# Kernel optimization log

Measured on AMD Instinct MI355X. Metric: run time of the kernel, lower is better.

Reference implementation:

```python
import jax, jax.numpy as jnp
import numpy as np

B, S, D = 32, 8192, 64


def setup_inputs() -> dict:
    key = jax.random.key(0)
    k1, k2 = jax.random.split(key)
    input_real = jax.random.normal(k1, (B, S, D), dtype=jnp.float32)
    input_imag = jax.random.normal(k2, (B, S, D), dtype=jnp.float32)
    return {"input_real": input_real, "input_imag": input_imag}


def reference(input_real, input_imag):
    # ComplexMixture: mean over seq of per-token complex outer products v v^H.
    # Original builds [B,S,D,D] via 4 batch_dots then means over S; fused here
    # as Gram contractions over the sequence axis (no [B,S,D,D] intermediate).
    seq_len = input_real.shape[1]
    inv_s = jnp.asarray(1.0 / seq_len, dtype=input_real.dtype)
    rr = jnp.einsum('bsi,bsj->bij', input_real, input_real)
    ii = jnp.einsum('bsi,bsj->bij', input_imag, input_imag)
    ri = jnp.einsum('bsi,bsj->bij', input_real, input_imag)
    out_real = (rr + ii) * inv_s                     # [B, D, D], symmetric
    out_imag = (ri - jnp.swapaxes(ri, 1, 2)) * inv_s  # [B, D, D], antisymmetric
    return (out_real, out_imag)
```

## Files before the change

kernel.cpp:

```cpp
#include <hip/hip_runtime.h>


#define BATCH  32
#define SEQ    8192
#define DD     64
#define CHUNKS 32
#define SCHUNK (SEQ / CHUNKS)
#define TR     64
#define NIT    (SCHUNK / TR)

typedef __bf16 bf16x8 __attribute__((ext_vector_type(8)));
typedef float  f32x16 __attribute__((ext_vector_type(16)));
typedef float  f32x4  __attribute__((ext_vector_type(4)));

__device__ __forceinline__ unsigned bf16pk(float a, float b) {
  unsigned ua = __builtin_bit_cast(unsigned, a);
  unsigned ub = __builtin_bit_cast(unsigned, b);
  ua = (ua + 0x7fffu + ((ua >> 16) & 1u)) >> 16;
  ub = (ub + 0x7fffu + ((ub >> 16) & 1u)) >> 16;
  return (ua & 0xffffu) | (ub << 16);
}

__device__ __forceinline__ int permd(int d) {
  return d ^ ((d >> 3) & 1) ^ (((d >> 4) & 1) << 1);
}

__device__ __forceinline__ void atomAdd(float* p, float v) {
  __hip_atomic_fetch_add(p, v, __ATOMIC_RELAXED, __HIP_MEMORY_SCOPE_AGENT);
}

__global__ __launch_bounds__(256, 4) void gram_fused(
    const float* __restrict__ R, const float* __restrict__ I,
    float* __restrict__ out)
{
  __shared__ uint4 lds[2][2][8][64];
  const int tid  = threadIdx.x;
  const int wave = tid >> 6;
  const int lane = tid & 63;
  const int l31  = lane & 31;
  const int lhi  = lane >> 5;
  const int mat  = tid >> 7;
  const int g    = (tid >> 4) & 7;
  const int q    = tid & 15;
  const int b = blockIdx.x & 31;
  const int c = blockIdx.x >> 5;
  const float* Mb = (mat ? I : R) + (size_t)b * (SEQ * DD);
  const int m0 = (wave >> 1) * 32;
  const int n0 = (wave & 1) * 32;
  const int pa = permd(m0 + l31);
  const int pb = permd(n0 + l31);
  int pw[4];
  #pragma unroll
  for (int cc = 0; cc < 4; ++cc) pw[cc] = permd(q * 4 + cc);

  f32x16 accR = {};
  f32x16 accI = {};

  f32x4 v[8];
  const size_t rbase = (size_t)(c * SCHUNK + g * 8) * DD;

#define LOADT(t_) do { \
    const f32x4* p_ = (const f32x4*)(Mb + rbase + (size_t)(t_) * TR * DD) + q; \
    _Pragma("unroll") \
    for (int j = 0; j < 8; ++j) v[j] = p_[j * 16]; \
    asm volatile("" ::: "memory"); \
  } while (0)

#define PACKW(buf_) do { \
    _Pragma("unroll") \
    for (int cc = 0; cc < 4; ++cc) { \
      uint4 u_; \
      u_.x = bf16pk(v[0][cc], v[1][cc]); u_.y = bf16pk(v[2][cc], v[3][cc]); \
      u_.z = bf16pk(v[4][cc], v[5][cc]); u_.w = bf16pk(v[6][cc], v[7][cc]); \
      lds[buf_][mat][g][pw[cc]] = u_; \
    } \
  } while (0)

#define TILEBAR() do { \
    __builtin_amdgcn_sched_barrier(0); \
    asm volatile("s_waitcnt lgkmcnt(0)" ::: "memory"); \
    __builtin_amdgcn_s_barrier(); \
    __builtin_amdgcn_sched_barrier(0); \
  } while (0)

  LOADT(0);
  PACKW(0);
  TILEBAR();

  #pragma unroll
  for (int it = 0; it < NIT; ++it) {
    const int buf = it & 1;
    if (it + 1 < NIT) LOADT(it + 1);
    #pragma unroll
    for (int ks = 0; ks < TR / 16; ++ks) {
      const int kg = ks * 2 + lhi;
      bf16x8 aR = __builtin_bit_cast(bf16x8, lds[buf][0][kg][pa]);
      bf16x8 bR = __builtin_bit_cast(bf16x8, lds[buf][0][kg][pb]);
      bf16x8 aI = __builtin_bit_cast(bf16x8, lds[buf][1][kg][pa]);
      bf16x8 bI = __builtin_bit_cast(bf16x8, lds[buf][1][kg][pb]);
      accR = __builtin_amdgcn_mfma_f32_32x32x16_bf16(aR, bR, accR, 0, 0, 0);
      accR = __builtin_amdgcn_mfma_f32_32x32x16_bf16(aI, bI, accR, 0, 0, 0);
      accI = __builtin_amdgcn_mfma_f32_32x32x16_bf16(aR, bI, accI, 0, 0, 0);
    }
    if (it + 1 < NIT) {
      PACKW(buf ^ 1);
      TILEBAR();
    }
  }
#undef LOADT
#undef PACKW
#undef TILEBAR

  const float inv = 1.0f / (float)SEQ;
  float* outR = out + (size_t)b * 4096;
  float* outM = out + 131072 + (size_t)b * 4096;
  const int jj = n0 + l31;

  #pragma unroll
  for (int r = 0; r < 16; ++r) {
    const int i = m0 + (r & 3) + 8 * (r >> 2) + 4 * lhi;
    atomAdd(&outR[i * 64 + jj], accR[r] * inv);
  }

  __syncthreads();
  float* sc = (float*)lds;
  #pragma unroll
  for (int r = 0; r < 16; ++r) {
    const int i = m0 + (r & 3) + 8 * (r >> 2) + 4 * lhi;
    sc[i * 65 + jj] = accI[r];
  }
  __syncthreads();
  #pragma unroll
  for (int r = 0; r < 16; ++r) {
    const int i = m0 + (r & 3) + 8 * (r >> 2) + 4 * lhi;
    const float m = (sc[i * 65 + jj] - sc[jj * 65 + i]) * inv;
    atomAdd(&outM[i * 64 + jj], m);
  }
}

extern "C" void kernel_launch(void* const* d_in, const int* in_sizes, int n_in,
                              void* d_out, int out_size, void* d_ws, size_t ws_size,
                              hipStream_t stream) {
  const float* R = (const float*)d_in[0];
  const float* I = (const float*)d_in[1];
  float* out = (float*)d_out;
  (void)d_ws; (void)ws_size;

  hipMemsetAsync(d_out, 0, (size_t)out_size, stream);
  gram_fused<<<BATCH * CHUNKS, 256, 0, stream>>>(R, I, out);
}
```

Baseline: 158.3 us.

## Deepen global-load prefetch to three tiles and halve sequence chunks

Raises register prefetch depth from one to three tiles ahead with a four-slot LDS ring, and halves the number of sequence chunks per batch so each block runs twice as many iterations. Occupancy hint drops from 4 to 2 blocks per CU to make room for the extra registers and LDS. The aim is more memory-level parallelism per wave to hide global load latency in this bandwidth-bound Gram reduction, plus fewer blocks and half as many output atomics. The risks are lower occupancy, higher register pressure, and fewer blocks (512) to spread across the GPU.

```diff
diff --git a/kernel.cpp b/kernel.cpp
--- a/kernel.cpp
+++ b/kernel.cpp
@@ -4,7 +4,7 @@
 #define BATCH  32
 #define SEQ    8192
 #define DD     64
-#define CHUNKS 32
+#define CHUNKS 16
 #define SCHUNK (SEQ / CHUNKS)
 #define TR     64
 #define NIT    (SCHUNK / TR)
@@ -29,11 +29,11 @@
   __hip_atomic_fetch_add(p, v, __ATOMIC_RELAXED, __HIP_MEMORY_SCOPE_AGENT);
 }
 
-__global__ __launch_bounds__(256, 4) void gram_fused(
+__global__ __launch_bounds__(256, 2) void gram_fused(
     const float* __restrict__ R, const float* __restrict__ I,
     float* __restrict__ out)
 {
-  __shared__ uint4 lds[2][2][8][64];
+  __shared__ uint4 lds[4][2][8][64];
   const int tid  = threadIdx.x;
   const int wave = tid >> 6;
   const int lane = tid & 63;
@@ -56,22 +56,24 @@
   f32x16 accR = {};
   f32x16 accI = {};
 
-  f32x4 v[8];
+  f32x4 v[3][8];
   const size_t rbase = (size_t)(c * SCHUNK + g * 8) * DD;
 
-#define LOADT(t_) do { \
+#define LOADT(t_, rs_) do { \
     const f32x4* p_ = (const f32x4*)(Mb + rbase + (size_t)(t_) * TR * DD) + q; \
     _Pragma("unroll") \
-    for (int j = 0; j < 8; ++j) v[j] = p_[j * 16]; \
+    for (int j = 0; j < 8; ++j) v[rs_][j] = p_[j * 16]; \
     asm volatile("" ::: "memory"); \
   } while (0)
 
-#define PACKW(buf_) do { \
+#define PACKW(buf_, rs_) do { \
     _Pragma("unroll") \
     for (int cc = 0; cc < 4; ++cc) { \
       uint4 u_; \
-      u_.x = bf16pk(v[0][cc], v[1][cc]); u_.y = bf16pk(v[2][cc], v[3][cc]); \
-      u_.z = bf16pk(v[4][cc], v[5][cc]); u_.w = bf16pk(v[6][cc], v[7][cc]); \
+      u_.x = bf16pk(v[rs_][0][cc], v[rs_][1][cc]); \
+      u_.y = bf16pk(v[rs_][2][cc], v[rs_][3][cc]); \
+      u_.z = bf16pk(v[rs_][4][cc], v[rs_][5][cc]); \
+      u_.w = bf16pk(v[rs_][6][cc], v[rs_][7][cc]); \
       lds[buf_][mat][g][pw[cc]] = u_; \
     } \
   } while (0)
@@ -83,14 +85,16 @@
     __builtin_amdgcn_sched_barrier(0); \
   } while (0)
 
-  LOADT(0);
-  PACKW(0);
+  LOADT(0, 0);
+  LOADT(1, 1);
+  LOADT(2, 2);
+  PACKW(0, 0);
   TILEBAR();
 
   #pragma unroll
-  for (int it = 0; it < NIT; ++it) {
-    const int buf = it & 1;
-    if (it + 1 < NIT) LOADT(it + 1);
+  for (int t = 0; t < NIT; ++t) {
+    if (t + 3 < NIT) LOADT(t + 3, (t + 3) % 3);
+    const int buf = t & 3;
     #pragma unroll
     for (int ks = 0; ks < TR / 16; ++ks) {
       const int kg = ks * 2 + lhi;
@@ -102,8 +106,8 @@
       accR = __builtin_amdgcn_mfma_f32_32x32x16_bf16(aI, bI, accR, 0, 0, 0);
       accI = __builtin_amdgcn_mfma_f32_32x32x16_bf16(aR, bI, accI, 0, 0, 0);
     }
-    if (it + 1 < NIT) {
-      PACKW(buf ^ 1);
+    if (t + 1 < NIT) {
+      PACKW((t + 1) & 3, (t + 1) % 3);
       TILEBAR();
     }
   }
```

Result: faster. 149.1 us (-5.8%).

## Load MFMA operands directly from global memory, dropping the LDS staging

Applied to the files above, without the earlier changes.

Each wave now reads its A and B fragments as scalar fp32 loads straight from global memory, packs them into bf16 registers, and feeds the MFMAs through a two-step register double buffer. The LDS tile staging, the swizzle and the per-tile barriers are gone. The aim is to remove LDS round trips and synchronisation, at the cost of redundant global and L2 reads, since each element is loaded by several waves and lanes. It also swaps coalesced 16-byte vector loads for strided 4-byte ones and raises register pressure.

```diff
diff --git a/kernel.cpp b/kernel.cpp
--- a/kernel.cpp
+++ b/kernel.cpp
@@ -6,12 +6,10 @@
 #define DD     64
 #define CHUNKS 32
 #define SCHUNK (SEQ / CHUNKS)
-#define TR     64
-#define NIT    (SCHUNK / TR)
+#define KST    (SCHUNK / 16)
 
 typedef __bf16 bf16x8 __attribute__((ext_vector_type(8)));
 typedef float  f32x16 __attribute__((ext_vector_type(16)));
-typedef float  f32x4  __attribute__((ext_vector_type(4)));
 
 __device__ __forceinline__ unsigned bf16pk(float a, float b) {
   unsigned ua = __builtin_bit_cast(unsigned, a);
@@ -19,10 +17,6 @@
   ua = (ua + 0x7fffu + ((ua >> 16) & 1u)) >> 16;
   ub = (ub + 0x7fffu + ((ub >> 16) & 1u)) >> 16;
   return (ua & 0xffffu) | (ub << 16);
-}
-
-__device__ __forceinline__ int permd(int d) {
-  return d ^ ((d >> 3) & 1) ^ (((d >> 4) & 1) << 1);
 }
 
 __device__ __forceinline__ void atomAdd(float* p, float v) {
@@ -33,83 +27,62 @@
     const float* __restrict__ R, const float* __restrict__ I,
     float* __restrict__ out)
 {
-  __shared__ uint4 lds[2][2][8][64];
+  __shared__ float sc[64 * 65];
   const int tid  = threadIdx.x;
   const int wave = tid >> 6;
   const int lane = tid & 63;
   const int l31  = lane & 31;
   const int lhi  = lane >> 5;
-  const int mat  = tid >> 7;
-  const int g    = (tid >> 4) & 7;
-  const int q    = tid & 15;
   const int b = blockIdx.x & 31;
   const int c = blockIdx.x >> 5;
-  const float* Mb = (mat ? I : R) + (size_t)b * (SEQ * DD);
   const int m0 = (wave >> 1) * 32;
   const int n0 = (wave & 1) * 32;
-  const int pa = permd(m0 + l31);
-  const int pb = permd(n0 + l31);
-  int pw[4];
-  #pragma unroll
-  for (int cc = 0; cc < 4; ++cc) pw[cc] = permd(q * 4 + cc);
+  const float* RbC = R + (size_t)b * (SEQ * DD) + (size_t)c * SCHUNK * DD;
+  const float* IbC = I + (size_t)b * (SEQ * DD) + (size_t)c * SCHUNK * DD;
+  const int offA = lhi * 8 * DD + m0 + l31;
+  const int offB = lhi * 8 * DD + n0 + l31;
 
   f32x16 accR = {};
   f32x16 accI = {};
 
-  f32x4 v[8];
-  const size_t rbase = (size_t)(c * SCHUNK + g * 8) * DD;
+  float ar[2][8], br[2][8], ai[2][8], bi[2][8];
 
-#define LOADT(t_) do { \
-    const f32x4* p_ = (const f32x4*)(Mb + rbase + (size_t)(t_) * TR * DD) + q; \
+#define LOADF(t_, rs_) do { \
+    const float* pR_ = RbC + (t_) * (16 * DD); \
+    const float* pI_ = IbC + (t_) * (16 * DD); \
     _Pragma("unroll") \
-    for (int j = 0; j < 8; ++j) v[j] = p_[j * 16]; \
+    for (int j = 0; j < 8; ++j) { \
+      ar[rs_][j] = pR_[offA + j * DD]; br[rs_][j] = pR_[offB + j * DD]; \
+      ai[rs_][j] = pI_[offA + j * DD]; bi[rs_][j] = pI_[offB + j * DD]; \
+    } \
     asm volatile("" ::: "memory"); \
   } while (0)
 
-#define PACKW(buf_) do { \
-    _Pragma("unroll") \
-    for (int cc = 0; cc < 4; ++cc) { \
-      uint4 u_; \
-      u_.x = bf16pk(v[0][cc], v[1][cc]); u_.y = bf16pk(v[2][cc], v[3][cc]); \
-      u_.z = bf16pk(v[4][cc], v[5][cc]); u_.w = bf16pk(v[6][cc], v[7][cc]); \
-      lds[buf_][mat][g][pw[cc]] = u_; \
-    } \
+#define CONV(rs_, fa_, arr_) do { \
+    uint4 u_; \
+    u_.x = bf16pk(arr_[rs_][0], arr_[rs_][1]); \
+    u_.y = bf16pk(arr_[rs_][2], arr_[rs_][3]); \
+    u_.z = bf16pk(arr_[rs_][4], arr_[rs_][5]); \
+    u_.w = bf16pk(arr_[rs_][6], arr_[rs_][7]); \
+    fa_ = __builtin_bit_cast(bf16x8, u_); \
   } while (0)
 
-#define TILEBAR() do { \
-    __builtin_amdgcn_sched_barrier(0); \
-    asm volatile("s_waitcnt lgkmcnt(0)" ::: "memory"); \
-    __builtin_amdgcn_s_barrier(); \
-    __builtin_amdgcn_sched_barrier(0); \
-  } while (0)
-
-  LOADT(0);
-  PACKW(0);
-  TILEBAR();
+  LOADF(0, 0);
+  LOADF(1, 1);
 
   #pragma unroll
-  for (int it = 0; it < NIT; ++it) {
-    const int buf = it & 1;
-    if (it + 1 < NIT) LOADT(it + 1);
-    #pragma unroll
-    for (int ks = 0; ks < TR / 16; ++ks) {
-      const int kg = ks * 2 + lhi;
-      bf16x8 aR = __builtin_bit_cast(bf16x8, lds[buf][0][kg][pa]);
-      bf16x8 bR = __builtin_bit_cast(bf16x8, lds[buf][0][kg][pb]);
-      bf16x8 aI = __builtin_bit_cast(bf16x8, lds[buf][1][kg][pa]);
-      bf16x8 bI = __builtin_bit_cast(bf16x8, lds[buf][1][kg][pb]);
-      accR = __builtin_amdgcn_mfma_f32_32x32x16_bf16(aR, bR, accR, 0, 0, 0);
-      accR = __builtin_amdgcn_mfma_f32_32x32x16_bf16(aI, bI, accR, 0, 0, 0);
-      accI = __builtin_amdgcn_mfma_f32_32x32x16_bf16(aR, bI, accI, 0, 0, 0);
-    }
-    if (it + 1 < NIT) {
-      PACKW(buf ^ 1);
-      TILEBAR();
-    }
+  for (int t = 0; t < KST; ++t) {
+    const int rs = t & 1;
+    bf16x8 faR, fbR, faI, fbI;
+    CONV(rs, faR, ar); CONV(rs, fbR, br);
+    CONV(rs, faI, ai); CONV(rs, fbI, bi);
+    if (t + 2 < KST) LOADF(t + 2, rs);
+    accR = __builtin_amdgcn_mfma_f32_32x32x16_bf16(faR, fbR, accR, 0, 0, 0);
+    accR = __builtin_amdgcn_mfma_f32_32x32x16_bf16(faI, fbI, accR, 0, 0, 0);
+    accI = __builtin_amdgcn_mfma_f32_32x32x16_bf16(faR, fbI, accI, 0, 0, 0);
   }
-#undef LOADT
-#undef PACKW
-#undef TILEBAR
+#undef LOADF
+#undef CONV
 
   const float inv = 1.0f / (float)SEQ;
   float* outR = out + (size_t)b * 4096;
@@ -122,8 +95,6 @@
     atomAdd(&outR[i * 64 + jj], accR[r] * inv);
   }
 
-  __syncthreads();
-  float* sc = (float*)lds;
   #pragma unroll
   for (int r = 0; r < 16; ++r) {
     const int i = m0 + (r & 3) + 8 * (r >> 2) + 4 * lhi;
```

Measured after the change: 266.7 us. 68.5% more time.
